# Optimization experiments

Measured on AMD Instinct MI355X. Metric: run time of the kernel, lower is better.

Reference implementation:

```python
import jax, jax.numpy as jnp
import numpy as np

B, T, E, D = 8, 2048, 1024, 128


def setup_inputs() -> dict:
    key = jax.random.key(0)
    k1, k2, k3, k4 = jax.random.split(key, 4)
    x = jax.random.normal(k1, (B, T, E), dtype=jnp.float32)
    wq = jax.random.normal(k2, (E, D), dtype=jnp.float32) * (E ** -0.5)
    wk = jax.random.normal(k3, (E, D), dtype=jnp.float32) * (E ** -0.5)
    wv = jax.random.normal(k4, (E, D), dtype=jnp.float32) * (E ** -0.5)
    return {"x": x, "wq": wq, "wk": wk, "wv": wv}


def reference(x, wq, wk, wv):
    # Projections (bias-free Linear): [B,T,E] @ [E,D] -> [B,T,D]
    q = x @ wq
    k = x @ wk
    v = x @ wv
    d = k.shape[-1]
    # Faithful to source: scores / d**(-0.5) == scores * sqrt(d)
    scores = jnp.einsum('btd,bsd->bts', q, k) * (d ** 0.5)
    causal = jnp.tril(jnp.ones((x.shape[1], x.shape[1]), dtype=bool))
    scores = jnp.where(causal, scores, -jnp.inf)
    weights = jax.nn.softmax(scores, axis=-1)  # dropout omitted (eval mode)
    return jnp.einsum('bts,bsd->btd', weights, v)
```

## Files before the change

### kernel.cpp

```cpp
#include <hip/hip_runtime.h>


#define NB 8
#define NT 2048
#define NE 1024
#define ND 128
#define NM (NB * NT)

typedef unsigned short U16;
typedef unsigned int U32;
typedef __attribute__((ext_vector_type(8))) short vbf8;
typedef __attribute__((ext_vector_type(4))) float vf4;

__device__ __forceinline__ U16 f2bf(float f) {
  U32 u = __builtin_bit_cast(U32, f);
  u += 0x7fffu + ((u >> 16) & 1u);
  return (U16)(u >> 16);
}
__device__ __forceinline__ float bf2f(U16 h) {
  U32 u = ((U32)h) << 16;
  return __builtin_bit_cast(float, u);
}
__device__ __forceinline__ void gl_lds16(const void* g, void* l) {
  __builtin_amdgcn_global_load_lds((__attribute__((address_space(1))) void*)g,
                                   (__attribute__((address_space(3))) void*)l, 16, 0, 0);
}

__global__ void wsplit_kernel(const float* __restrict__ wq, const float* __restrict__ wk,
                              const float* __restrict__ wv, U16* __restrict__ wth,
                              U16* __restrict__ wtl) {
  int id = blockIdx.x * 256 + threadIdx.x;
  if (id >= 384 * 1024) return;
  int n = id >> 10, e = id & 1023;
  float v;
  if (n < 128)      v = wq[e * 128 + n] * 11.313708498984761f;
  else if (n < 256) v = wk[e * 128 + (n - 128)];
  else              v = wv[e * 128 + (n - 256)];
  U16 h = f2bf(v);
  wth[id] = h;
  wtl[id] = f2bf(v - bf2f(h));
}

__global__ __launch_bounds__(256, 3) void qkv_kernel(
    const float* __restrict__ x, const U16* __restrict__ wth, const U16* __restrict__ wtl,
    U16* __restrict__ qh, U16* __restrict__ ql, U16* __restrict__ kh, U16* __restrict__ kl,
    U16* __restrict__ vt) {
  __shared__ __align__(16) char smem[49152];
  char* Ah = smem;
  char* Al = smem + 8192;
  char* Bh = smem + 16384;
  char* Bl = smem + 32768;

  const int tid = threadIdx.x;
  const int w = tid >> 6, lane = tid & 63;
  const int fr = lane & 15, fq = lane >> 4;
  const int m0 = blockIdx.x * 64;
  const int nt = blockIdx.y;
  const U16* bh_src = wth + nt * (128 * 1024);
  const U16* bl_src = wtl + nt * (128 * 1024);

  const vf4 vzero = {0.f, 0.f, 0.f, 0.f};
  vf4 acc[2][4];
#pragma unroll
  for (int i = 0; i < 2; ++i)
#pragma unroll
    for (int j = 0; j < 4; ++j) acc[i][j] = vzero;

  const int wm = (w >> 1) * 32, wn = (w & 1) * 64;
  const int arow = tid >> 2, ag = tid & 3;

  for (int k0 = 0; k0 < 1024; k0 += 64) {
#pragma unroll
    for (int p = 0; p < 4; ++p) {
      const int g = p * 256 + tid;
      const int row = g >> 3, c = g & 7;
      const int sc = c ^ (row & 7);
      const int ldsb = (p * 256 + w * 64) * 16;
      gl_lds16(bh_src + row * 1024 + k0 + sc * 8, Bh + ldsb);
      if (nt < 2) gl_lds16(bl_src + row * 1024 + k0 + sc * 8, Bl + ldsb);
    }
    {
      const float* s = x + (size_t)(m0 + arow) * 1024 + k0 + ag * 8;
      float v0[8], v1[8];
      ((float4*)v0)[0] = *(const float4*)(s);
      ((float4*)v0)[1] = *(const float4*)(s + 4);
      ((float4*)v1)[0] = *(const float4*)(s + 32);
      ((float4*)v1)[1] = *(const float4*)(s + 36);
      vbf8 h0, l0, h1, l1;
#pragma unroll
      for (int i = 0; i < 8; ++i) {
        U16 a = f2bf(v0[i]);
        h0[i] = (short)a; l0[i] = (short)f2bf(v0[i] - bf2f(a));
        U16 b = f2bf(v1[i]);
        h1[i] = (short)b; l1[i] = (short)f2bf(v1[i] - bf2f(b));
      }
      const int sw = arow & 7;
      *(vbf8*)(Ah + arow * 128 + ((ag ^ sw) << 4))       = h0;
      *(vbf8*)(Ah + arow * 128 + (((ag + 4) ^ sw) << 4)) = h1;
      if (nt < 2) {
        *(vbf8*)(Al + arow * 128 + ((ag ^ sw) << 4))       = l0;
        *(vbf8*)(Al + arow * 128 + (((ag + 4) ^ sw) << 4)) = l1;
      }
    }
    __syncthreads();

    if (nt < 2) {
#pragma unroll
      for (int kc = 0; kc < 2; ++kc) {
        vbf8 a_h[2], a_l[2], b_h[4], b_l[4];
#pragma unroll
        for (int i = 0; i < 2; ++i) {
          const int row = wm + i * 16 + fr;
          const int off = row * 128 + (((kc * 4 + fq) ^ (row & 7)) << 4);
          a_h[i] = *(const vbf8*)(Ah + off);
          a_l[i] = *(const vbf8*)(Al + off);
        }
#pragma unroll
        for (int j = 0; j < 4; ++j) {
          const int row = wn + j * 16 + fr;
          const int off = row * 128 + (((kc * 4 + fq) ^ (row & 7)) << 4);
          b_h[j] = *(const vbf8*)(Bh + off);
          b_l[j] = *(const vbf8*)(Bl + off);
        }
#pragma unroll
        for (int i = 0; i < 2; ++i)
#pragma unroll
          for (int j = 0; j < 4; ++j) {
            acc[i][j] = __builtin_amdgcn_mfma_f32_16x16x32_bf16(a_h[i], b_h[j], acc[i][j], 0, 0, 0);
            acc[i][j] = __builtin_amdgcn_mfma_f32_16x16x32_bf16(a_h[i], b_l[j], acc[i][j], 0, 0, 0);
            acc[i][j] = __builtin_amdgcn_mfma_f32_16x16x32_bf16(a_l[i], b_h[j], acc[i][j], 0, 0, 0);
          }
      }
    } else {
#pragma unroll
      for (int kc = 0; kc < 2; ++kc) {
        vbf8 a_h[2], b_h[4];
#pragma unroll
        for (int i = 0; i < 2; ++i) {
          const int row = wm + i * 16 + fr;
          a_h[i] = *(const vbf8*)(Ah + row * 128 + (((kc * 4 + fq) ^ (row & 7)) << 4));
        }
#pragma unroll
        for (int j = 0; j < 4; ++j) {
          const int row = wn + j * 16 + fr;
          b_h[j] = *(const vbf8*)(Bh + row * 128 + (((kc * 4 + fq) ^ (row & 7)) << 4));
        }
#pragma unroll
        for (int i = 0; i < 2; ++i)
#pragma unroll
          for (int j = 0; j < 4; ++j)
            acc[i][j] = __builtin_amdgcn_mfma_f32_16x16x32_bf16(a_h[i], b_h[j], acc[i][j], 0, 0, 0);
      }
    }
    __syncthreads();
  }

  if (nt < 2) {
    U16* dh = (nt == 0) ? qh : kh;
    U16* dl = (nt == 0) ? ql : kl;
#pragma unroll
    for (int i = 0; i < 2; ++i)
#pragma unroll
      for (int j = 0; j < 4; ++j)
#pragma unroll
        for (int r = 0; r < 4; ++r) {
          const int row = m0 + wm + i * 16 + fq * 4 + r;
          const int col = wn + j * 16 + fr;
          const float val = acc[i][j][r];
          const U16 h = f2bf(val);
          dh[row * 128 + col] = h;
          dl[row * 128 + col] = f2bf(val - bf2f(h));
        }
  } else {
    U16* tl = (U16*)smem;
#pragma unroll
    for (int i = 0; i < 2; ++i)
#pragma unroll
      for (int j = 0; j < 4; ++j)
#pragma unroll
        for (int r = 0; r < 4; ++r) {
          const int ml = wm + i * 16 + fq * 4 + r;
          const int col = wn + j * 16 + fr;
          tl[col * 80 + ml] = f2bf(acc[i][j][r]);
        }
    __syncthreads();
    const int bb = m0 >> 11, t0 = m0 & 2047;
#pragma unroll
    for (int p = 0; p < 4; ++p) {
      const int g = p * 256 + tid;
      const int d = g >> 3, c = g & 7;
      *(vbf8*)(vt + (size_t)(bb * 128 + d) * 2048 + t0 + c * 8) = *(const vbf8*)(tl + d * 80 + c * 8);
    }
  }
}

__global__ __launch_bounds__(256) void flash_kernel(
    const U16* __restrict__ qh, const U16* __restrict__ ql, const U16* __restrict__ kh,
    const U16* __restrict__ kl, const U16* __restrict__ vt, float* __restrict__ out) {
  __shared__ __align__(16) char smem[54272];
  U16* Kh = (U16*)smem;
  U16* Kl = (U16*)(smem + 16384);
  U16* Vt = (U16*)(smem + 32768);
  U16* Pl = (U16*)(smem + 49152);

  const int tid = threadIdx.x;
  const int w = tid >> 6, lane = tid & 63;
  const int fr = lane & 15, fq = lane >> 4;
  const int bid = blockIdx.x;
  const int bb = bid & 7;
  const int jj = bid >> 3;
  const int qt = (bid < 256) ? (63 - jj) : (jj - 32);
  const int q0 = qt * 32;
  const int pairI = w >> 1;
  const int wrow = (w & 1) * 16;

  vbf8 q_h[4], q_l[4];
  {
    const int rg = (bb * 2048 + q0 + wrow + fr) * 128 + fq * 8;
#pragma unroll
    for (int kc = 0; kc < 4; ++kc) {
      q_h[kc] = *(const vbf8*)(qh + rg + kc * 32);
      q_l[kc] = *(const vbf8*)(ql + rg + kc * 32);
    }
  }

  const vf4 vzero = {0.f, 0.f, 0.f, 0.f};
  vf4 oacc[8];
#pragma unroll
  for (int i = 0; i < 8; ++i) oacc[i] = vzero;
  float m_r[4], l_r[4];
#pragma unroll
  for (int r = 0; r < 4; ++r) { m_r[r] = -__builtin_inff(); l_r[r] = 0.f; }

  const int nlast = (qt + 2) >> 1;
  for (int ntile = 0; ntile < nlast; ++ntile) {
    const int s0 = ntile * 64;
#pragma unroll
    for (int p = 0; p < 4; ++p) {
      const int g = p * 256 + tid;
      const int lb = (p * 256 + w * 64) * 8;
      {
        const int s = g >> 4, c = g & 15;
        const int cl = c ^ (s & 7);
        const int src = (bb * 2048 + s0 + s) * 128 + cl * 8;
        gl_lds16(kh + src, Kh + lb);
        gl_lds16(kl + src, Kl + lb);
      }
      {
        const int d = g >> 3, c = g & 7;
        const int cv = c ^ (d & 7);
        gl_lds16(vt + (bb * 128 + d) * 2048 + s0 + cv * 8, Vt + lb);
      }
    }
    __syncthreads();

    vf4 sacc[2] = {vzero, vzero};
    __builtin_amdgcn_s_setprio(1);
#pragma unroll
    for (int nf = 0; nf < 2; ++nf) {
      const int s_loc = pairI * 32 + nf * 16 + fr;
      const int swz = (s_loc & 7) << 4;
#pragma unroll
      for (int kc = 0; kc < 4; ++kc) {
        const int off = ((s_loc * 256 + kc * 64 + fq * 16) ^ swz) >> 1;
        vbf8 kfh = *(const vbf8*)(Kh + off);
        vbf8 kfl = *(const vbf8*)(Kl + off);
        sacc[nf] = __builtin_amdgcn_mfma_f32_16x16x32_bf16(q_h[kc], kfh, sacc[nf], 0, 0, 0);
        sacc[nf] = __builtin_amdgcn_mfma_f32_16x16x32_bf16(q_h[kc], kfl, sacc[nf], 0, 0, 0);
        sacc[nf] = __builtin_amdgcn_mfma_f32_16x16x32_bf16(q_l[kc], kfh, sacc[nf], 0, 0, 0);
      }
    }
    __builtin_amdgcn_s_setprio(0);

    if (ntile == nlast - 1) {
#pragma unroll
      for (int nf = 0; nf < 2; ++nf) {
        const int s_g = s0 + pairI * 32 + nf * 16 + fr;
#pragma unroll
        for (int r = 0; r < 4; ++r) {
          const int q_g = q0 + wrow + fq * 4 + r;
          if (s_g > q_g) sacc[nf][r] = -__builtin_inff();
        }
      }
    }

    float tmax[4];
#pragma unroll
    for (int r = 0; r < 4; ++r) tmax[r] = fmaxf(sacc[0][r], sacc[1][r]);
#pragma unroll
    for (int off = 1; off < 16; off <<= 1)
#pragma unroll
      for (int r = 0; r < 4; ++r) tmax[r] = fmaxf(tmax[r], __shfl_xor(tmax[r], off, 64));

    float alpha[4], mne[4];
#pragma unroll
    for (int r = 0; r < 4; ++r) {
      const float mn = fmaxf(m_r[r], tmax[r]);
      mne[r] = (mn == -__builtin_inff()) ? 0.f : mn;
      alpha[r] = __expf(m_r[r] - mne[r]);
      m_r[r] = mn;
    }

    float psum[4] = {0.f, 0.f, 0.f, 0.f};
    U16 pb[2][4];
#pragma unroll
    for (int nf = 0; nf < 2; ++nf)
#pragma unroll
      for (int r = 0; r < 4; ++r) {
        const float pv = __expf(sacc[nf][r] - mne[r]);
        psum[r] += pv;
        pb[nf][r] = f2bf(pv);
      }
#pragma unroll
    for (int off = 1; off < 16; off <<= 1)
#pragma unroll
      for (int r = 0; r < 4; ++r) psum[r] += __shfl_xor(psum[r], off, 64);
#pragma unroll
    for (int r = 0; r < 4; ++r) l_r[r] = l_r[r] * alpha[r] + psum[r];
#pragma unroll
    for (int i = 0; i < 8; ++i)
#pragma unroll
      for (int r = 0; r < 4; ++r) oacc[i][r] *= alpha[r];

    U16* pw = Pl + w * (16 * 40);
#pragma unroll
    for (int nf = 0; nf < 2; ++nf)
#pragma unroll
      for (int r = 0; r < 4; ++r) pw[(fq * 4 + r) * 40 + nf * 16 + fr] = pb[nf][r];
    asm volatile("s_waitcnt lgkmcnt(0)" ::: "memory");
    const vbf8 pf = *(const vbf8*)(pw + fr * 40 + fq * 8);
    __builtin_amdgcn_s_setprio(1);
#pragma unroll
    for (int i = 0; i < 8; ++i) {
      const int d_loc = i * 16 + fr;
      const int off = ((d_loc * 128 + (pairI * 32 + fq * 8) * 2) ^ ((d_loc & 7) << 4)) >> 1;
      const vbf8 vfr = *(const vbf8*)(Vt + off);
      oacc[i] = __builtin_amdgcn_mfma_f32_16x16x32_bf16(pf, vfr, oacc[i], 0, 0, 0);
    }
    __builtin_amdgcn_s_setprio(0);
    __syncthreads();
  }

  float* O_l = (float*)smem;
  float* m_l = (float*)(smem + 16384);
  float* l_l = (float*)(smem + 16384 + 256);
  if (pairI == 1) {
#pragma unroll
    for (int i = 0; i < 8; ++i)
#pragma unroll
      for (int r = 0; r < 4; ++r)
        O_l[(wrow + fq * 4 + r) * 128 + i * 16 + fr] = oacc[i][r];
    if (fr == 0) {
#pragma unroll
      for (int r = 0; r < 4; ++r) {
        m_l[wrow + fq * 4 + r] = m_r[r];
        l_l[wrow + fq * 4 + r] = l_r[r];
      }
    }
  }
  __syncthreads();
  if (pairI == 0) {
    float aA[4], aB[4], inv[4];
#pragma unroll
    for (int r = 0; r < 4; ++r) {
      const int row = wrow + fq * 4 + r;
      const float mB = m_l[row], lB = l_l[row];
      const float M = fmaxf(m_r[r], mB);
      aA[r] = __expf(m_r[r] - M);
      aB[r] = __expf(mB - M);
      inv[r] = 1.f / (l_r[r] * aA[r] + lB * aB[r]);
    }
#pragma unroll
    for (int i = 0; i < 8; ++i)
#pragma unroll
      for (int r = 0; r < 4; ++r) {
        const int row = wrow + fq * 4 + r;
        out[(bb * 2048 + q0 + row) * 128 + i * 16 + fr] =
            (oacc[i][r] * aA[r] + O_l[row * 128 + i * 16 + fr] * aB[r]) * inv[r];
      }
  }
}

extern "C" void kernel_launch(void* const* d_in, const int* in_sizes, int n_in, void* d_out,
                              int out_size, void* d_ws, size_t ws_size, hipStream_t stream) {
  const float* x = (const float*)d_in[0];
  const float* wq = (const float*)d_in[1];
  const float* wk = (const float*)d_in[2];
  const float* wv = (const float*)d_in[3];
  char* ws = (char*)d_ws;
  U16* wth = (U16*)(ws);
  U16* wtl = (U16*)(ws + 786432);
  U16* qh  = (U16*)(ws + 1572864);
  U16* ql  = (U16*)(ws + 5767168);
  U16* kh  = (U16*)(ws + 9961472);
  U16* kl  = (U16*)(ws + 14155776);
  U16* vt  = (U16*)(ws + 18350080);
  float* out = (float*)d_out;

  wsplit_kernel<<<dim3(1536), dim3(256), 0, stream>>>(wq, wk, wv, wth, wtl);
  qkv_kernel<<<dim3(256, 3), dim3(256), 0, stream>>>(x, wth, wtl, qh, ql, kh, kl, vt);
  flash_kernel<<<dim3(512), dim3(256), 0, stream>>>(qh, ql, kh, kl, vt, out);
}
```

Before: 114.3 us.

## Split KV range across waves with 16-row query tiles and direct global loads

```diff
diff --git a/kernel.cpp b/kernel.cpp
--- a/kernel.cpp
+++ b/kernel.cpp
@@ -194,29 +194,24 @@
   }
 }
 
-__global__ __launch_bounds__(256) void flash_kernel(
+__global__ __launch_bounds__(256, 4) void flash_kernel(
     const U16* __restrict__ qh, const U16* __restrict__ ql, const U16* __restrict__ kh,
     const U16* __restrict__ kl, const U16* __restrict__ vt, float* __restrict__ out) {
-  __shared__ __align__(16) char smem[54272];
-  U16* Kh = (U16*)smem;
-  U16* Kl = (U16*)(smem + 16384);
-  U16* Vt = (U16*)(smem + 32768);
-  U16* Pl = (U16*)(smem + 49152);
+  __shared__ __align__(16) char smem[33280];
 
   const int tid = threadIdx.x;
   const int w = tid >> 6, lane = tid & 63;
   const int fr = lane & 15, fq = lane >> 4;
   const int bid = blockIdx.x;
   const int bb = bid & 7;
-  const int jj = bid >> 3;
-  const int qt = (bid < 256) ? (63 - jj) : (jj - 32);
-  const int q0 = qt * 32;
-  const int pairI = w >> 1;
-  const int wrow = (w & 1) * 16;
+  const int j = bid >> 3;
+  const int kk = j >> 5, gm = j & 31;
+  const int g = (kk == 0) ? gm : (kk == 1) ? (63 - gm) : (kk == 2) ? (64 + gm) : (127 - gm);
+  const int q0 = g * 16;
 
   vbf8 q_h[4], q_l[4];
   {
-    const int rg = (bb * 2048 + q0 + wrow + fr) * 128 + fq * 8;
+    const int rg = (bb * 2048 + q0 + fr) * 128 + fq * 8;
 #pragma unroll
     for (int kc = 0; kc < 4; ++kc) {
       q_h[kc] = *(const vbf8*)(qh + rg + kc * 32);
@@ -224,6 +219,11 @@
     }
   }
 
+  const U16* kh_b = kh + (size_t)bb * 2048 * 128 + fr * 128 + fq * 8;
+  const U16* kl_b = kl + (size_t)bb * 2048 * 128 + fr * 128 + fq * 8;
+  const U16* vt_b = vt + (size_t)bb * 128 * 2048 + fr * 2048 + fq * 8;
+  U16* pw = (U16*)(smem + w * 2304);
+
   const vf4 vzero = {0.f, 0.f, 0.f, 0.f};
   vf4 oacc[8];
 #pragma unroll
@@ -232,53 +232,32 @@
 #pragma unroll
   for (int r = 0; r < 4; ++r) { m_r[r] = -__builtin_inff(); l_r[r] = 0.f; }
 
-  const int nlast = (qt + 2) >> 1;
-  for (int ntile = 0; ntile < nlast; ++ntile) {
-    const int s0 = ntile * 64;
-#pragma unroll
-    for (int p = 0; p < 4; ++p) {
-      const int g = p * 256 + tid;
-      const int lb = (p * 256 + w * 64) * 8;
-      {
-        const int s = g >> 4, c = g & 15;
-        const int cl = c ^ (s & 7);
-        const int src = (bb * 2048 + s0 + s) * 128 + cl * 8;
-        gl_lds16(kh + src, Kh + lb);
-        gl_lds16(kl + src, Kl + lb);
-      }
-      {
-        const int d = g >> 3, c = g & 7;
-        const int cv = c ^ (d & 7);
-        gl_lds16(vt + (bb * 128 + d) * 2048 + s0 + cv * 8, Vt + lb);
-      }
-    }
-    __syncthreads();
-
-    vf4 sacc[2] = {vzero, vzero};
-    __builtin_amdgcn_s_setprio(1);
-#pragma unroll
-    for (int nf = 0; nf < 2; ++nf) {
-      const int s_loc = pairI * 32 + nf * 16 + fr;
-      const int swz = (s_loc & 7) << 4;
+  const int ntiles = (q0 + 79) >> 6;
+  for (int t = w; t < ntiles; t += 4) {
+    const int s0 = t * 64;
+
+    vf4 sacc[4] = {vzero, vzero, vzero, vzero};
+#pragma unroll
+    for (int nf = 0; nf < 4; ++nf) {
+      const U16* kh_t = kh_b + (s0 + nf * 16) * 128;
+      const U16* kl_t = kl_b + (s0 + nf * 16) * 128;
 #pragma unroll
       for (int kc = 0; kc < 4; ++kc) {
-        const int off = ((s_loc * 256 + kc * 64 + fq * 16) ^ swz) >> 1;
-        vbf8 kfh = *(const vbf8*)(Kh + off);
-        vbf8 kfl = *(const vbf8*)(Kl + off);
+        const vbf8 kfh = *(const vbf8*)(kh_t + kc * 32);
+        const vbf8 kfl = *(const vbf8*)(kl_t + kc * 32);
         sacc[nf] = __builtin_amdgcn_mfma_f32_16x16x32_bf16(q_h[kc], kfh, sacc[nf], 0, 0, 0);
         sacc[nf] = __builtin_amdgcn_mfma_f32_16x16x32_bf16(q_h[kc], kfl, sacc[nf], 0, 0, 0);
         sacc[nf] = __builtin_amdgcn_mfma_f32_16x16x32_bf16(q_l[kc], kfh, sacc[nf], 0, 0, 0);
       }
     }
-    __builtin_amdgcn_s_setprio(0);
-
-    if (ntile == nlast - 1) {
-#pragma unroll
-      for (int nf = 0; nf < 2; ++nf) {
-        const int s_g = s0 + pairI * 32 + nf * 16 + fr;
+
+    if (s0 + 63 > q0) {
+#pragma unroll
+      for (int nf = 0; nf < 4; ++nf) {
+        const int s_g = s0 + nf * 16 + fr;
 #pragma unroll
         for (int r = 0; r < 4; ++r) {
-          const int q_g = q0 + wrow + fq * 4 + r;
+          const int q_g = q0 + fq * 4 + r;
           if (s_g > q_g) sacc[nf][r] = -__builtin_inff();
         }
       }
@@ -286,7 +265,8 @@
 
     float tmax[4];
 #pragma unroll
-    for (int r = 0; r < 4; ++r) tmax[r] = fmaxf(sacc[0][r], sacc[1][r]);
+    for (int r = 0; r < 4; ++r)
+      tmax[r] = fmaxf(fmaxf(sacc[0][r], sacc[1][r]), fmaxf(sacc[2][r], sacc[3][r]));
 #pragma unroll
     for (int off = 1; off < 16; off <<= 1)
 #pragma unroll
@@ -302,9 +282,9 @@
     }
 
     float psum[4] = {0.f, 0.f, 0.f, 0.f};
-    U16 pb[2][4];
-#pragma unroll
-    for (int nf = 0; nf < 2; ++nf)
+    U16 pb[4][4];
+#pragma unroll
+    for (int nf = 0; nf < 4; ++nf)
 #pragma unroll
       for (int r = 0; r < 4; ++r) {
         const float pv = __expf(sacc[nf][r] - mne[r]);
@@ -322,63 +302,63 @@
 #pragma unroll
       for (int r = 0; r < 4; ++r) oacc[i][r] *= alpha[r];
 
-    U16* pw = Pl + w * (16 * 40);
-#pragma unroll
-    for (int nf = 0; nf < 2; ++nf)
-#pragma unroll
-      for (int r = 0; r < 4; ++r) pw[(fq * 4 + r) * 40 + nf * 16 + fr] = pb[nf][r];
+#pragma unroll
+    for (int nf = 0; nf < 4; ++nf)
+#pragma unroll
+      for (int r = 0; r < 4; ++r) pw[(fq * 4 + r) * 72 + nf * 16 + fr] = pb[nf][r];
     asm volatile("s_waitcnt lgkmcnt(0)" ::: "memory");
-    const vbf8 pf = *(const vbf8*)(pw + fr * 40 + fq * 8);
-    __builtin_amdgcn_s_setprio(1);
+    const vbf8 pf0 = *(const vbf8*)(pw + fr * 72 + fq * 8);
+    const vbf8 pf1 = *(const vbf8*)(pw + fr * 72 + 32 + fq * 8);
+
 #pragma unroll
     for (int i = 0; i < 8; ++i) {
-      const int d_loc = i * 16 + fr;
-      const int off = ((d_loc * 128 + (pairI * 32 + fq * 8) * 2) ^ ((d_loc & 7) << 4)) >> 1;
-      const vbf8 vfr = *(const vbf8*)(Vt + off);
-      oacc[i] = __builtin_amdgcn_mfma_f32_16x16x32_bf16(pf, vfr, oacc[i], 0, 0, 0);
-    }
-    __builtin_amdgcn_s_setprio(0);
-    __syncthreads();
-  }
-
-  float* O_l = (float*)smem;
-  float* m_l = (float*)(smem + 16384);
-  float* l_l = (float*)(smem + 16384 + 256);
-  if (pairI == 1) {
-#pragma unroll
-    for (int i = 0; i < 8; ++i)
-#pragma unroll
-      for (int r = 0; r < 4; ++r)
-        O_l[(wrow + fq * 4 + r) * 128 + i * 16 + fr] = oacc[i][r];
-    if (fr == 0) {
-#pragma unroll
-      for (int r = 0; r < 4; ++r) {
-        m_l[wrow + fq * 4 + r] = m_r[r];
-        l_l[wrow + fq * 4 + r] = l_r[r];
-      }
-    }
-  }
+      const vbf8 v0 = *(const vbf8*)(vt_b + i * 16 * 2048 + s0);
+      const vbf8 v1 = *(const vbf8*)(vt_b + i * 16 * 2048 + s0 + 32);
+      oacc[i] = __builtin_amdgcn_mfma_f32_16x16x32_bf16(pf0, v0, oacc[i], 0, 0, 0);
+      oacc[i] = __builtin_amdgcn_mfma_f32_16x16x32_bf16(pf1, v1, oacc[i], 0, 0, 0);
+    }
+  }
+
   __syncthreads();
-  if (pairI == 0) {
-    float aA[4], aB[4], inv[4];
+  float* O_p = (float*)smem;
+  float* m_s = (float*)(smem + 32768);
+  float* l_s = (float*)(smem + 33024);
+#pragma unroll
+  for (int i = 0; i < 8; ++i)
+#pragma unroll
+    for (int r = 0; r < 4; ++r)
+      O_p[(w * 16 + fq * 4 + r) * 128 + i * 16 + fr] = oacc[i][r];
+  if (fr == 0) {
 #pragma unroll
     for (int r = 0; r < 4; ++r) {
-      const int row = wrow + fq * 4 + r;
-      const float mB = m_l[row], lB = l_l[row];
-      const float M = fmaxf(m_r[r], mB);
-      aA[r] = __expf(m_r[r] - M);
-      aB[r] = __expf(mB - M);
-      inv[r] = 1.f / (l_r[r] * aA[r] + lB * aB[r]);
-    }
-#pragma unroll
-    for (int i = 0; i < 8; ++i)
-#pragma unroll
-      for (int r = 0; r < 4; ++r) {
-        const int row = wrow + fq * 4 + r;
-        out[(bb * 2048 + q0 + row) * 128 + i * 16 + fr] =
-            (oacc[i][r] * aA[r] + O_l[row * 128 + i * 16 + fr] * aB[r]) * inv[r];
-      }
-  }
+      m_s[w * 16 + fq * 4 + r] = m_r[r];
+      l_s[w * 16 + fq * 4 + r] = l_r[r];
+    }
+  }
+  __syncthreads();
+
+  const int row = tid >> 4, cg = tid & 15;
+  float mv[4];
+  float M = -__builtin_inff();
+#pragma unroll
+  for (int p = 0; p < 4; ++p) { mv[p] = m_s[p * 16 + row]; M = fmaxf(M, mv[p]); }
+  float wgt[4], wsum = 0.f;
+#pragma unroll
+  for (int p = 0; p < 4; ++p) {
+    wgt[p] = __expf(mv[p] - M);
+    wsum += wgt[p] * l_s[p * 16 + row];
+  }
+  const float inv = 1.f / wsum;
+  float o[8];
+#pragma unroll
+  for (int c = 0; c < 8; ++c) o[c] = 0.f;
+#pragma unroll
+  for (int p = 0; p < 4; ++p)
+#pragma unroll
+    for (int c = 0; c < 8; ++c) o[c] += wgt[p] * O_p[(p * 16 + row) * 128 + cg * 8 + c];
+#pragma unroll
+  for (int c = 0; c < 8; ++c)
+    out[(size_t)(bb * 2048 + q0 + row) * 128 + cg * 8 + c] = o[c] * inv;
 }
 
 extern "C" void kernel_launch(void* const* d_in, const int* in_sizes, int n_in, void* d_out,
@@ -399,5 +379,5 @@
 
   wsplit_kernel<<<dim3(1536), dim3(256), 0, stream>>>(wq, wk, wv, wth, wtl);
   qkv_kernel<<<dim3(256, 3), dim3(256), 0, stream>>>(x, wth, wtl, qh, ql, kh, kl, vt);
-  flash_kernel<<<dim3(512), dim3(256), 0, stream>>>(qh, ql, kh, kl, vt, out);
-}
+  flash_kernel<<<dim3(1024), dim3(256), 0, stream>>>(qh, ql, kh, kl, vt, out);
+}
```

Result: slower. 149.9 us (+31.1%).

## Split flash attention KV tile across four waves per query group with 512 threads

Applied to the files above, without the earlier changes.

```diff
diff --git a/kernel.cpp b/kernel.cpp
--- a/kernel.cpp
+++ b/kernel.cpp
@@ -194,29 +194,36 @@
   }
 }
 
-__global__ __launch_bounds__(256) void flash_kernel(
+__global__ __launch_bounds__(512, 4) void flash_kernel(
     const U16* __restrict__ qh, const U16* __restrict__ ql, const U16* __restrict__ kh,
     const U16* __restrict__ kl, const U16* __restrict__ vt, float* __restrict__ out) {
-  __shared__ __align__(16) char smem[54272];
-  U16* Kh = (U16*)smem;
-  U16* Kl = (U16*)(smem + 16384);
-  U16* Vt = (U16*)(smem + 32768);
-  U16* Pl = (U16*)(smem + 49152);
+  __shared__ __align__(16) char smem[59392];
+  char* KhB = smem;
+  char* KlB = smem + 16384;
+  char* Vt  = smem + 32768;
 
   const int tid = threadIdx.x;
   const int w = tid >> 6, lane = tid & 63;
   const int fr = lane & 15, fq = lane >> 4;
+  const int qg = w >> 2, sq = w & 3;
   const int bid = blockIdx.x;
   const int bb = bid & 7;
   const int jj = bid >> 3;
   const int qt = (bid < 256) ? (63 - jj) : (jj - 32);
   const int q0 = qt * 32;
-  const int pairI = w >> 1;
-  const int wrow = (w & 1) * 16;
+  const int nt = (qt + 2) >> 1;
+
+  const U16* khb = kh + (size_t)bb * 2048 * 128;
+  const U16* klb = kl + (size_t)bb * 2048 * 128;
+  const U16* vtb = vt + (size_t)bb * 128 * 2048;
+  U16* pw = (U16*)(smem + 49152 + w * 1280);
+
+  *(U32*)(pw + fr * 40 + 16 + fq * 4) = 0u;
+  *(U32*)(pw + fr * 40 + 18 + fq * 4) = 0u;
 
   vbf8 q_h[4], q_l[4];
   {
-    const int rg = (bb * 2048 + q0 + wrow + fr) * 128 + fq * 8;
+    const int rg = (bb * 2048 + q0 + qg * 16 + fr) * 128 + fq * 8;
 #pragma unroll
     for (int kc = 0; kc < 4; ++kc) {
       q_h[kc] = *(const vbf8*)(qh + rg + kc * 32);
@@ -224,6 +231,16 @@
     }
   }
 
+  const int kr0 = tid >> 4;
+  const int kg0 = tid & 15;
+  const int ksc0 = ((kg0 ^ (kr0 & 7)) * 8);
+  const int kr1 = 32 + kr0;
+  const int ksc1 = ((kg0 ^ (kr1 & 7)) * 8);
+  const int vd0 = tid >> 3;
+  const int vsc0 = (((tid & 7) ^ (vd0 & 7)) * 8);
+  const int vd1 = 64 + vd0;
+  const int vsc1 = (((tid & 7) ^ (vd1 & 7)) * 8);
+
   const vf4 vzero = {0.f, 0.f, 0.f, 0.f};
   vf4 oacc[8];
 #pragma unroll
@@ -232,61 +249,44 @@
 #pragma unroll
   for (int r = 0; r < 4; ++r) { m_r[r] = -__builtin_inff(); l_r[r] = 0.f; }
 
-  const int nlast = (qt + 2) >> 1;
-  for (int ntile = 0; ntile < nlast; ++ntile) {
-    const int s0 = ntile * 64;
-#pragma unroll
-    for (int p = 0; p < 4; ++p) {
-      const int g = p * 256 + tid;
-      const int lb = (p * 256 + w * 64) * 8;
-      {
-        const int s = g >> 4, c = g & 15;
-        const int cl = c ^ (s & 7);
-        const int src = (bb * 2048 + s0 + s) * 128 + cl * 8;
-        gl_lds16(kh + src, Kh + lb);
-        gl_lds16(kl + src, Kl + lb);
-      }
-      {
-        const int d = g >> 3, c = g & 7;
-        const int cv = c ^ (d & 7);
-        gl_lds16(vt + (bb * 128 + d) * 2048 + s0 + cv * 8, Vt + lb);
-      }
-    }
+  const int s_loc = sq * 16 + fr;
+  const int kswz = (s_loc & 7) << 4;
+
+  for (int t = 0; t < nt; ++t) {
+    const int s0 = t * 64;
+    gl_lds16(khb + (size_t)(s0 + kr0) * 128 + ksc0, KhB + w * 1024);
+    gl_lds16(khb + (size_t)(s0 + kr1) * 128 + ksc1, KhB + 8192 + w * 1024);
+    gl_lds16(klb + (size_t)(s0 + kr0) * 128 + ksc0, KlB + w * 1024);
+    gl_lds16(klb + (size_t)(s0 + kr1) * 128 + ksc1, KlB + 8192 + w * 1024);
+    gl_lds16(vtb + (size_t)vd0 * 2048 + s0 + vsc0, Vt + w * 1024);
+    gl_lds16(vtb + (size_t)vd1 * 2048 + s0 + vsc1, Vt + 8192 + w * 1024);
     __syncthreads();
 
-    vf4 sacc[2] = {vzero, vzero};
+    vf4 sacc = vzero;
     __builtin_amdgcn_s_setprio(1);
 #pragma unroll
-    for (int nf = 0; nf < 2; ++nf) {
-      const int s_loc = pairI * 32 + nf * 16 + fr;
-      const int swz = (s_loc & 7) << 4;
-#pragma unroll
-      for (int kc = 0; kc < 4; ++kc) {
-        const int off = ((s_loc * 256 + kc * 64 + fq * 16) ^ swz) >> 1;
-        vbf8 kfh = *(const vbf8*)(Kh + off);
-        vbf8 kfl = *(const vbf8*)(Kl + off);
-        sacc[nf] = __builtin_amdgcn_mfma_f32_16x16x32_bf16(q_h[kc], kfh, sacc[nf], 0, 0, 0);
-        sacc[nf] = __builtin_amdgcn_mfma_f32_16x16x32_bf16(q_h[kc], kfl, sacc[nf], 0, 0, 0);
-        sacc[nf] = __builtin_amdgcn_mfma_f32_16x16x32_bf16(q_l[kc], kfh, sacc[nf], 0, 0, 0);
-      }
+    for (int kc = 0; kc < 4; ++kc) {
+      const int off = (s_loc * 256 + kc * 64 + fq * 16) ^ kswz;
+      const vbf8 kfh = *(const vbf8*)(KhB + off);
+      const vbf8 kfl = *(const vbf8*)(KlB + off);
+      sacc = __builtin_amdgcn_mfma_f32_16x16x32_bf16(q_h[kc], kfh, sacc, 0, 0, 0);
+      sacc = __builtin_amdgcn_mfma_f32_16x16x32_bf16(q_h[kc], kfl, sacc, 0, 0, 0);
+      sacc = __builtin_amdgcn_mfma_f32_16x16x32_bf16(q_l[kc], kfh, sacc, 0, 0, 0);
     }
     __builtin_amdgcn_s_setprio(0);
 
-    if (ntile == nlast - 1) {
-#pragma unroll
-      for (int nf = 0; nf < 2; ++nf) {
-        const int s_g = s0 + pairI * 32 + nf * 16 + fr;
-#pragma unroll
-        for (int r = 0; r < 4; ++r) {
-          const int q_g = q0 + wrow + fq * 4 + r;
-          if (s_g > q_g) sacc[nf][r] = -__builtin_inff();
-        }
+    if (t == nt - 1) {
+      const int s_g = s0 + s_loc;
+#pragma unroll
+      for (int r = 0; r < 4; ++r) {
+        const int q_g = q0 + qg * 16 + fq * 4 + r;
+        if (s_g > q_g) sacc[r] = -__builtin_inff();
       }
     }
 
     float tmax[4];
 #pragma unroll
-    for (int r = 0; r < 4; ++r) tmax[r] = fmaxf(sacc[0][r], sacc[1][r]);
+    for (int r = 0; r < 4; ++r) tmax[r] = sacc[r];
 #pragma unroll
     for (int off = 1; off < 16; off <<= 1)
 #pragma unroll
@@ -301,16 +301,14 @@
       m_r[r] = mn;
     }
 
-    float psum[4] = {0.f, 0.f, 0.f, 0.f};
-    U16 pb[2][4];
-#pragma unroll
-    for (int nf = 0; nf < 2; ++nf)
-#pragma unroll
-      for (int r = 0; r < 4; ++r) {
-        const float pv = __expf(sacc[nf][r] - mne[r]);
-        psum[r] += pv;
-        pb[nf][r] = f2bf(pv);
-      }
+    float psum[4];
+    U16 pb[4];
+#pragma unroll
+    for (int r = 0; r < 4; ++r) {
+      const float pv = __expf(sacc[r] - mne[r]);
+      psum[r] = pv;
+      pb[r] = f2bf(pv);
+    }
 #pragma unroll
     for (int off = 1; off < 16; off <<= 1)
 #pragma unroll
@@ -322,62 +320,70 @@
 #pragma unroll
       for (int r = 0; r < 4; ++r) oacc[i][r] *= alpha[r];
 
-    U16* pw = Pl + w * (16 * 40);
-#pragma unroll
-    for (int nf = 0; nf < 2; ++nf)
-#pragma unroll
-      for (int r = 0; r < 4; ++r) pw[(fq * 4 + r) * 40 + nf * 16 + fr] = pb[nf][r];
+#pragma unroll
+    for (int r = 0; r < 4; ++r) pw[(fq * 4 + r) * 40 + fr] = pb[r];
     asm volatile("s_waitcnt lgkmcnt(0)" ::: "memory");
     const vbf8 pf = *(const vbf8*)(pw + fr * 40 + fq * 8);
+
+    const int s_v = (sq * 16 + fq * 8) & 63;
     __builtin_amdgcn_s_setprio(1);
 #pragma unroll
     for (int i = 0; i < 8; ++i) {
       const int d_loc = i * 16 + fr;
-      const int off = ((d_loc * 128 + (pairI * 32 + fq * 8) * 2) ^ ((d_loc & 7) << 4)) >> 1;
+      const int off = (d_loc * 128 + s_v * 2) ^ ((d_loc & 7) << 4);
       const vbf8 vfr = *(const vbf8*)(Vt + off);
       oacc[i] = __builtin_amdgcn_mfma_f32_16x16x32_bf16(pf, vfr, oacc[i], 0, 0, 0);
     }
     __builtin_amdgcn_s_setprio(0);
-    __syncthreads();
-  }
-
-  float* O_l = (float*)smem;
-  float* m_l = (float*)(smem + 16384);
-  float* l_l = (float*)(smem + 16384 + 256);
-  if (pairI == 1) {
+    __builtin_amdgcn_s_barrier();
+  }
+
+  __syncthreads();
+  float* O_d = (float*)smem;
+  float* m_s = (float*)(smem + 49152);
+  float* l_s = (float*)(smem + 49664);
+  if (sq > 0) {
 #pragma unroll
     for (int i = 0; i < 8; ++i)
 #pragma unroll
       for (int r = 0; r < 4; ++r)
-        O_l[(wrow + fq * 4 + r) * 128 + i * 16 + fr] = oacc[i][r];
-    if (fr == 0) {
-#pragma unroll
-      for (int r = 0; r < 4; ++r) {
-        m_l[wrow + fq * 4 + r] = m_r[r];
-        l_l[wrow + fq * 4 + r] = l_r[r];
-      }
+        O_d[((qg * 3 + sq - 1) * 16 + fq * 4 + r) * 128 + i * 16 + fr] = oacc[i][r];
+  }
+  if (fr == 0) {
+#pragma unroll
+    for (int r = 0; r < 4; ++r) {
+      m_s[(qg * 4 + sq) * 16 + fq * 4 + r] = m_r[r];
+      l_s[(qg * 4 + sq) * 16 + fq * 4 + r] = l_r[r];
     }
   }
   __syncthreads();
-  if (pairI == 0) {
-    float aA[4], aB[4], inv[4];
+  if (sq == 0) {
 #pragma unroll
     for (int r = 0; r < 4; ++r) {
-      const int row = wrow + fq * 4 + r;
-      const float mB = m_l[row], lB = l_l[row];
-      const float M = fmaxf(m_r[r], mB);
-      aA[r] = __expf(m_r[r] - M);
-      aB[r] = __expf(mB - M);
-      inv[r] = 1.f / (l_r[r] * aA[r] + lB * aB[r]);
-    }
-#pragma unroll
-    for (int i = 0; i < 8; ++i)
-#pragma unroll
-      for (int r = 0; r < 4; ++r) {
-        const int row = wrow + fq * 4 + r;
-        out[(bb * 2048 + q0 + row) * 128 + i * 16 + fr] =
-            (oacc[i][r] * aA[r] + O_l[row * 128 + i * 16 + fr] * aB[r]) * inv[r];
-      }
+      const int row = fq * 4 + r;
+      float mv[4];
+      float M = -__builtin_inff();
+#pragma unroll
+      for (int p = 0; p < 4; ++p) {
+        mv[p] = m_s[(qg * 4 + p) * 16 + row];
+        M = fmaxf(M, mv[p]);
+      }
+      float wgt[4], denom = 0.f;
+#pragma unroll
+      for (int p = 0; p < 4; ++p) {
+        wgt[p] = __expf(mv[p] - M);
+        denom += wgt[p] * l_s[(qg * 4 + p) * 16 + row];
+      }
+      const float inv = 1.f / denom;
+#pragma unroll
+      for (int i = 0; i < 8; ++i) {
+        float o = wgt[0] * oacc[i][r];
+#pragma unroll
+        for (int p = 1; p < 4; ++p)
+          o += wgt[p] * O_d[((qg * 3 + p - 1) * 16 + row) * 128 + i * 16 + fr];
+        out[(size_t)(bb * 2048 + q0 + qg * 16 + row) * 128 + i * 16 + fr] = o * inv;
+      }
+    }
   }
 }
 
@@ -399,5 +405,5 @@
 
   wsplit_kernel<<<dim3(1536), dim3(256), 0, stream>>>(wq, wk, wv, wth, wtl);
   qkv_kernel<<<dim3(256, 3), dim3(256), 0, stream>>>(x, wth, wtl, qh, ql, kh, kl, vt);
-  flash_kernel<<<dim3(512), dim3(256), 0, stream>>>(qh, ql, kh, kl, vt, out);
-}
+  flash_kernel<<<dim3(512), dim3(512), 0, stream>>>(qh, ql, kh, kl, vt, out);
+}
```

New measurement: 127.9 us. 11.8% more time.
